# Kernel tuning notes

Measured on AMD Instinct MI355X. Metric: run time of the kernel, lower is better.

Reference implementation:

```python
import jax, jax.numpy as jnp
import numpy as np

B, S, IN, HID = 16, 4096, 512, 512
NH = 4
HD = HID // NH            # 128
NA = 4 * 2                # num_attractors*2 = 8 codes per head
EPS = 1e-5


def _ln(x, g, b):
    m = jnp.mean(x, axis=-1, keepdims=True)
    v = jnp.mean((x - m) ** 2, axis=-1, keepdims=True)
    return (x - m) * jax.lax.rsqrt(v + EPS) * g + b


def setup_inputs() -> dict:
    key = jax.random.key(0)
    ks = jax.random.split(key, 16)
    d = {
        "x": jax.random.normal(ks[0], (B, S, IN), jnp.float32),
        "norm_g": jnp.ones((IN,), jnp.float32),
        "norm_b": jnp.zeros((IN,), jnp.float32),
        # per-head MLP (stacked over head axis h)
        "hW1": jax.random.normal(ks[1], (NH, IN, 2 * HD), jnp.float32) / np.sqrt(IN).astype(np.float32),
        "hb1": jnp.zeros((NH, 2 * HD), jnp.float32),
        "hln_g": jnp.ones((NH, 2 * HD), jnp.float32),
        "hln_b": jnp.zeros((NH, 2 * HD), jnp.float32),
        "hW2": jax.random.normal(ks[2], (NH, 2 * HD, HD), jnp.float32) / np.sqrt(2 * HD).astype(np.float32),
        "hb2": jnp.zeros((NH, HD), jnp.float32),
        # attractor codebooks, dynamics, gates
        "attractors": jax.random.normal(ks[3], (NH, NA, HD), jnp.float32) / np.sqrt(HD).astype(np.float32),
        "dynamics": jnp.eye(HD, dtype=jnp.float32)[None] + 0.05 * jax.random.normal(ks[4], (NH, HD, HD), jnp.float32),
        "gW": jax.random.normal(ks[5], (NH, IN), jnp.float32) / np.sqrt(IN).astype(np.float32),
        "gb": jnp.zeros((NH,), jnp.float32),
        # output MLP
        "oW1": jax.random.normal(ks[6], (HID, HID), jnp.float32) / np.sqrt(HID).astype(np.float32),
        "ob1": jnp.zeros((HID,), jnp.float32),
        "oln_g": jnp.ones((HID,), jnp.float32),
        "oln_b": jnp.zeros((HID,), jnp.float32),
        "oW2": jax.random.normal(ks[7], (HID, IN), jnp.float32) / np.sqrt(HID).astype(np.float32),
        "ob2": jnp.zeros((IN,), jnp.float32),
    }
    return d


def reference(x, norm_g, norm_b, hW1, hb1, hln_g, hln_b, hW2, hb2,
              attractors, dynamics, gW, gb, oW1, ob1, oln_g, oln_b, oW2, ob2):
    xn = _ln(x, norm_g, norm_b)
    # per-head MLP (dropout is identity in eval): [B,S,NH,2HD] -> [B,S,NH,HD]
    h = jnp.einsum("bsi,hio->bsho", xn, hW1) + hb1
    h = jax.nn.gelu(_ln(h, hln_g, hln_b), approximate=False)
    state = jnp.einsum("bsho,hod->bshd", h, hW2) + hb2
    # cdist to tiny codebook via ||s||^2 + ||a||^2 - 2 s.a (matches torch.cdist matmul mode)
    s2 = jnp.sum(state * state, axis=-1, keepdims=True)          # [B,S,NH,1]
    a2 = jnp.sum(attractors * attractors, axis=-1)               # [NH,NA]
    sa = jnp.einsum("bshd,had->bsha", state, attractors)         # [B,S,NH,NA]
    dists = jnp.sqrt(jnp.maximum(s2 + a2 - 2.0 * sa, 0.0))
    attn = jax.nn.softmax(-dists / np.sqrt(HD).astype(np.float32), axis=-1)
    attr_infl = jnp.einsum("bsha,had->bshd", attn, attractors)
    dyn = jnp.einsum("bshd,hde->bshe", state, dynamics)
    gate = jax.nn.sigmoid(jnp.einsum("bsi,hi->bsh", xn, gW) + gb)[..., None]
    head_out = state + gate * 0.1 * (attr_infl - state + jnp.tanh(dyn))
    combined = head_out.reshape(*head_out.shape[:2], HID)        # concat heads
    o = combined @ oW1 + ob1
    o = jax.nn.gelu(_ln(o, oln_g, oln_b), approximate=False)
    o = o @ oW2 + ob2
    return xn + o
```

## Files before the change

### kernel.cpp

```cpp
#include <hip/hip_runtime.h>

typedef unsigned short u16;
typedef __bf16 bf16x8 __attribute__((ext_vector_type(8)));
typedef short  s16x8  __attribute__((ext_vector_type(8)));
typedef float  f32x4  __attribute__((ext_vector_type(4)));

template <bool B, class T, class F> struct cond_t { using type = T; };
template <class T, class F> struct cond_t<false, T, F> { using type = F; };
template <typename T>
__device__ auto probe_mfma(int)
    -> decltype(__builtin_amdgcn_mfma_f32_16x16x32_bf16(T{}, T{}, f32x4{}, 0, 0, 0), (char)0);
template <typename T> __device__ short probe_mfma(...);
using frag_t = typename cond_t<sizeof(probe_mfma<bf16x8>(0)) == 1, bf16x8, s16x8>::type;
#define MFMA(a, b, c) __builtin_amdgcn_mfma_f32_16x16x32_bf16((a), (b), (c), 0, 0, 0)

__device__ __forceinline__ float bf2f(u16 u) {
  unsigned int x = ((unsigned int)u) << 16; float f; __builtin_memcpy(&f, &x, 4); return f;
}
__device__ __forceinline__ u16 f2bf(float f) {
  unsigned int x; __builtin_memcpy(&x, &f, 4);
  x += 0x7fffu + ((x >> 16) & 1u);
  return (u16)(x >> 16);
}
__device__ __forceinline__ float fast_rcp(float x) { return __builtin_amdgcn_rcpf(x); }
__device__ __forceinline__ float tanh_fast(float x) {
  float t = __expf(2.0f * x);
  return 1.0f - 2.0f * fast_rcp(1.0f + t);
}
__device__ __forceinline__ float gelu_f(float x) {
  float x3 = x * x * x;
  return 0.5f * x * (1.0f + tanh_fast(0.7978845608028654f * x + 0.035677408136300125f * x3));
}
__device__ __forceinline__ float sigmoid_fast(float x) {
  return fast_rcp(1.0f + __expf(-x));
}

__global__ __launch_bounds__(256) void k_tr(const float* __restrict__ src, u16* __restrict__ dst,
                                            int batch, int K, int N) {
  long KN = (long)K * N;
  long total = (long)batch * KN;
  for (long i = (long)blockIdx.x * blockDim.x + threadIdx.x; i < total;
       i += (long)gridDim.x * blockDim.x) {
    long b = i / KN; long rem = i - b * KN;
    long n = rem / K; long k = rem - n * K;
    dst[i] = f2bf(src[b * KN + k * N + n]);
  }
}

__global__ __launch_bounds__(256) void k1_ln_gate(
    const float* __restrict__ x, const float* __restrict__ ng, const float* __restrict__ nb,
    const float* __restrict__ gW, const float* __restrict__ gb,
    u16* __restrict__ xn, float* __restrict__ gate) {
  const int lane = threadIdx.x & 63;
  const long t = (long)blockIdx.x * 4 + (threadIdx.x >> 6);
  float4 a0 = *(const float4*)(x + t * 512 + lane * 8);
  float4 a1 = *(const float4*)(x + t * 512 + lane * 8 + 4);
  float f[8] = {a0.x, a0.y, a0.z, a0.w, a1.x, a1.y, a1.z, a1.w};
  float s = 0.f, ss = 0.f;
#pragma unroll
  for (int j = 0; j < 8; j++) { s += f[j]; ss += f[j] * f[j]; }
#pragma unroll
  for (int m = 1; m < 64; m <<= 1) { s += __shfl_xor(s, m); ss += __shfl_xor(ss, m); }
  const float mean = s * (1.0f / 512.0f);
  const float rstd = rsqrtf(ss * (1.0f / 512.0f) - mean * mean + 1e-5f);
  float xf[8];
  union { uint4 q; u16 u[8]; } st;
#pragma unroll
  for (int j = 0; j < 8; j++) {
    xf[j] = (f[j] - mean) * rstd * ng[lane * 8 + j] + nb[lane * 8 + j];
    st.u[j] = f2bf(xf[j]);
  }
  *(uint4*)(xn + t * 512 + lane * 8) = st.q;
  for (int h = 0; h < 4; h++) {
    float p = 0.f;
#pragma unroll
    for (int j = 0; j < 8; j++) p += xf[j] * gW[h * 512 + lane * 8 + j];
#pragma unroll
    for (int m = 1; m < 64; m <<= 1) p += __shfl_xor(p, m);
    if (lane == 0) gate[t * 4 + h] = sigmoid_fast(p + gb[h]);
  }
}

__global__ __launch_bounds__(256, 1) void k2_head(
    const u16* __restrict__ xn, const u16* __restrict__ hW1t, const float* __restrict__ hb1,
    const float* __restrict__ hlng, const float* __restrict__ hlnb,
    const u16* __restrict__ hW2t, const float* __restrict__ hb2,
    const float* __restrict__ attr, const u16* __restrict__ dynT,
    const float* __restrict__ gate, u16* __restrict__ outC) {
  __shared__ __align__(16) char smem[44032];
  u16* sA  = (u16*)(smem);
  u16* sB  = (u16*)(smem + 5120);
  u16* sH  = (u16*)(smem);
  u16* sB2 = (u16*)(smem + 33792);
  u16* sSt = (u16*)(smem);
  float* sAttrF = (float*)(smem + 17408);
  float* sA2    = (float*)(smem + 21504);

  const int tid = threadIdx.x;
  const int lane = tid & 63, wv = tid >> 6, q = lane >> 4, l15 = lane & 15;
  const int h = blockIdx.y;
  const long t0 = (long)blockIdx.x * 64;
  const f32x4 vz = {0.f, 0.f, 0.f, 0.f};

  f32x4 acc[16];
#pragma unroll
  for (int i = 0; i < 16; i++) acc[i] = vz;
  const int arow = tid >> 2, ako = (tid & 3) * 8;

  for (int kb = 0; kb < 512; kb += 32) {
    *(uint4*)&sA[arow * 40 + ako] = *(const uint4*)&xn[(t0 + arow) * 512 + kb + ako];
#pragma unroll
    for (int i = 0; i < 4; i++) {
      int c = tid + 256 * i, r = c >> 2, ko = (c & 3) * 8;
      *(uint4*)&sB[r * 40 + ko] = *(const uint4*)&hW1t[((long)h * 256 + r) * 512 + kb + ko];
    }
    __syncthreads();
    frag_t af = *(const frag_t*)&sA[(wv * 16 + l15) * 40 + q * 8];
#pragma unroll
    for (int nt = 0; nt < 16; nt++) {
      frag_t bf = *(const frag_t*)&sB[(nt * 16 + l15) * 40 + q * 8];
      acc[nt] = MFMA(af, bf, acc[nt]);
    }
    __syncthreads();
  }

  {
    float bb[16], cg[16], cb[16];
#pragma unroll
    for (int nt = 0; nt < 16; nt++) {
      int col = nt * 16 + l15;
      bb[nt] = hb1[h * 256 + col];
      cg[nt] = hlng[h * 256 + col];
      cb[nt] = hlnb[h * 256 + col];
    }
#pragma unroll
    for (int r = 0; r < 4; r++) {
      float s = 0.f, ss = 0.f;
#pragma unroll
      for (int nt = 0; nt < 16; nt++) { float v = acc[nt][r] + bb[nt]; s += v; ss += v * v; }
#pragma unroll
      for (int m = 1; m < 16; m <<= 1) { s += __shfl_xor(s, m); ss += __shfl_xor(ss, m); }
      float mean = s * (1.f / 256.f);
      float rstd = rsqrtf(ss * (1.f / 256.f) - mean * mean + 1e-5f);
      int row = wv * 16 + q * 4 + r;
#pragma unroll
      for (int nt = 0; nt < 16; nt++) {
        float v = (acc[nt][r] + bb[nt] - mean) * rstd * cg[nt] + cb[nt];
        sH[row * 264 + nt * 16 + l15] = f2bf(gelu_f(v));
      }
    }
  }
  __syncthreads();

  f32x4 acc2[8];
#pragma unroll
  for (int i = 0; i < 8; i++) acc2[i] = vz;
  for (int kb = 0; kb < 256; kb += 32) {
#pragma unroll
    for (int i = 0; i < 2; i++) {
      int c = tid + 256 * i, r = c >> 2, ko = (c & 3) * 8;
      *(uint4*)&sB2[r * 40 + ko] = *(const uint4*)&hW2t[((long)h * 128 + r) * 256 + kb + ko];
    }
    __syncthreads();
    frag_t af = *(const frag_t*)&sH[(wv * 16 + l15) * 264 + kb + q * 8];
#pragma unroll
    for (int nt = 0; nt < 8; nt++) {
      frag_t bf = *(const frag_t*)&sB2[(nt * 16 + l15) * 40 + q * 8];
      acc2[nt] = MFMA(af, bf, acc2[nt]);
    }
    __syncthreads();
  }
#pragma unroll
  for (int nt = 0; nt < 8; nt++) {
    float b2 = hb2[h * 128 + nt * 16 + l15];
#pragma unroll
    for (int r = 0; r < 4; r++) acc2[nt][r] += b2;
  }

#pragma unroll
  for (int nt = 0; nt < 8; nt++)
#pragma unroll
    for (int r = 0; r < 4; r++)
      sSt[(wv * 16 + q * 4 + r) * 136 + nt * 16 + l15] = f2bf(acc2[nt][r]);
#pragma unroll
  for (int i = 0; i < 4; i++) { int c = tid + 256 * i; sAttrF[c] = attr[h * 1024 + c]; }
  __syncthreads();
  if (tid < 64) {
    int a = tid >> 3, j = tid & 7;
    float s = 0.f;
#pragma unroll
    for (int d2 = 0; d2 < 16; d2++) { float v = sAttrF[a * 128 + j * 16 + d2]; s += v * v; }
#pragma unroll
    for (int m = 1; m < 8; m <<= 1) s += __shfl_xor(s, m);
    if (j == 0) sA2[a] = s;
  }
  __syncthreads();

  f32x4 dacc[8];
#pragma unroll
  for (int i = 0; i < 8; i++) dacc[i] = vz;
  for (int kb = 0; kb < 128; kb += 32) {
#pragma unroll
    for (int i = 0; i < 2; i++) {
      int c = tid + 256 * i, r = c >> 2, ko = (c & 3) * 8;
      *(uint4*)&sB2[r * 40 + ko] = *(const uint4*)&dynT[((long)h * 128 + r) * 128 + kb + ko];
    }
    __syncthreads();
    frag_t af = *(const frag_t*)&sSt[(wv * 16 + l15) * 136 + kb + q * 8];
#pragma unroll
    for (int nt = 0; nt < 8; nt++) {
      frag_t bf = *(const frag_t*)&sB2[(nt * 16 + l15) * 40 + q * 8];
      dacc[nt] = MFMA(af, bf, dacc[nt]);
    }
    __syncthreads();
  }

  const float dscale = 0.088388347648318447f;
#pragma unroll
  for (int r = 0; r < 4; r++) {
    const long t = t0 + wv * 16 + q * 4 + r;
    float s2v = 0.f;
#pragma unroll
    for (int nt = 0; nt < 8; nt++) s2v += acc2[nt][r] * acc2[nt][r];
#pragma unroll
    for (int m = 1; m < 16; m <<= 1) s2v += __shfl_xor(s2v, m);
    float lg[8]; float mx = -3.0e38f;
#pragma unroll
    for (int a = 0; a < 8; a++) {
      float sa = 0.f;
#pragma unroll
      for (int nt = 0; nt < 8; nt++) sa += acc2[nt][r] * sAttrF[a * 128 + nt * 16 + l15];
#pragma unroll
      for (int m = 1; m < 16; m <<= 1) sa += __shfl_xor(sa, m);
      float dist = sqrtf(fmaxf(s2v + sA2[a] - 2.0f * sa, 0.0f));
      lg[a] = -dist * dscale;
      mx = fmaxf(mx, lg[a]);
    }
    float den = 0.f;
#pragma unroll
    for (int a = 0; a < 8; a++) { lg[a] = __expf(lg[a] - mx); den += lg[a]; }
    const float rden = fast_rcp(den);
    const float g01 = gate[t * 4 + h] * 0.1f;
#pragma unroll
    for (int nt = 0; nt < 8; nt++) {
      int col = nt * 16 + l15;
      float ai = 0.f;
#pragma unroll
      for (int a = 0; a < 8; a++) ai += lg[a] * sAttrF[a * 128 + col];
      ai *= rden;
      float stv = acc2[nt][r];
      float ho = stv + g01 * (ai - stv + tanh_fast(dacc[nt][r]));
      outC[t * 1024 + h * 128 + col] = f2bf(ho);
    }
  }
}

__global__ __launch_bounds__(256, 1) void k3_mlp1(
    const u16* __restrict__ inp, const u16* __restrict__ oW1t,
    const float* __restrict__ ob1, const float* __restrict__ olng, const float* __restrict__ olnb,
    u16* __restrict__ outp) {
  __shared__ __align__(16) char smem[46080];
  u16* sA = (u16*)smem;
  u16* sB = (u16*)(smem + 5120);
  const int tid = threadIdx.x, lane = tid & 63, wv = tid >> 6, q = lane >> 4, l15 = lane & 15;
  const long t0 = (long)blockIdx.x * 64;
  const f32x4 vz = {0.f, 0.f, 0.f, 0.f};
  f32x4 acc[32];
#pragma unroll
  for (int i = 0; i < 32; i++) acc[i] = vz;
  const int arow = tid >> 2, ako = (tid & 3) * 8;
  for (int kb = 0; kb < 512; kb += 32) {
    *(uint4*)&sA[arow * 40 + ako] = *(const uint4*)&inp[(t0 + arow) * 1024 + kb + ako];
#pragma unroll
    for (int i = 0; i < 8; i++) {
      int c = tid + 256 * i, r = c >> 2, ko = (c & 3) * 8;
      *(uint4*)&sB[r * 40 + ko] = *(const uint4*)&oW1t[(long)r * 512 + kb + ko];
    }
    __syncthreads();
    frag_t af = *(const frag_t*)&sA[(wv * 16 + l15) * 40 + q * 8];
#pragma unroll
    for (int nt = 0; nt < 32; nt++) {
      frag_t bf = *(const frag_t*)&sB[(nt * 16 + l15) * 40 + q * 8];
      acc[nt] = MFMA(af, bf, acc[nt]);
    }
    __syncthreads();
  }
  float bb[32];
#pragma unroll
  for (int nt = 0; nt < 32; nt++) bb[nt] = ob1[nt * 16 + l15];
#pragma unroll
  for (int r = 0; r < 4; r++) {
    float s = 0.f, ss = 0.f;
#pragma unroll
    for (int nt = 0; nt < 32; nt++) { float v = acc[nt][r] + bb[nt]; s += v; ss += v * v; }
#pragma unroll
    for (int m = 1; m < 16; m <<= 1) { s += __shfl_xor(s, m); ss += __shfl_xor(ss, m); }
    float mean = s * (1.f / 512.f);
    float rstd = rsqrtf(ss * (1.f / 512.f) - mean * mean + 1e-5f);
    const long t = t0 + wv * 16 + q * 4 + r;
#pragma unroll
    for (int nt = 0; nt < 32; nt++) {
      int col = nt * 16 + l15;
      float v = (acc[nt][r] + bb[nt] - mean) * rstd * olng[col] + olnb[col];
      outp[t * 1024 + col] = f2bf(gelu_f(v));
    }
  }
}

__global__ __launch_bounds__(256, 1) void k4_mlp2(
    const u16* __restrict__ inp, const u16* __restrict__ oW2t,
    const float* __restrict__ ob2, const u16* __restrict__ xn,
    float* __restrict__ outp) {
  __shared__ __align__(16) char smem[46080];
  u16* sA = (u16*)smem;
  u16* sB = (u16*)(smem + 5120);
  const int tid = threadIdx.x, lane = tid & 63, wv = tid >> 6, q = lane >> 4, l15 = lane & 15;
  const long t0 = (long)blockIdx.x * 64;
  const f32x4 vz = {0.f, 0.f, 0.f, 0.f};
  f32x4 acc[32];
#pragma unroll
  for (int i = 0; i < 32; i++) acc[i] = vz;
  const int arow = tid >> 2, ako = (tid & 3) * 8;
  for (int kb = 0; kb < 512; kb += 32) {
    *(uint4*)&sA[arow * 40 + ako] = *(const uint4*)&inp[(t0 + arow) * 1024 + kb + ako];
#pragma unroll
    for (int i = 0; i < 8; i++) {
      int c = tid + 256 * i, r = c >> 2, ko = (c & 3) * 8;
      *(uint4*)&sB[r * 40 + ko] = *(const uint4*)&oW2t[(long)r * 512 + kb + ko];
    }
    __syncthreads();
    frag_t af = *(const frag_t*)&sA[(wv * 16 + l15) * 40 + q * 8];
#pragma unroll
    for (int nt = 0; nt < 32; nt++) {
      frag_t bf = *(const frag_t*)&sB[(nt * 16 + l15) * 40 + q * 8];
      acc[nt] = MFMA(af, bf, acc[nt]);
    }
    __syncthreads();
  }
#pragma unroll
  for (int r = 0; r < 4; r++) {
    const long t = t0 + wv * 16 + q * 4 + r;
#pragma unroll
    for (int nt = 0; nt < 32; nt++) {
      int col = nt * 16 + l15;
      float v = acc[nt][r] + ob2[col] + bf2f(xn[t * 512 + col]);
      outp[t * 512 + col] = v;
    }
  }
}

extern "C" void kernel_launch(void* const* d_in, const int* in_sizes, int n_in,
                              void* d_out, int out_size, void* d_ws, size_t ws_size,
                              hipStream_t stream) {
  const float* x    = (const float*)d_in[0];
  const float* ng   = (const float*)d_in[1];
  const float* nbp  = (const float*)d_in[2];
  const float* hW1  = (const float*)d_in[3];
  const float* hb1  = (const float*)d_in[4];
  const float* hlng = (const float*)d_in[5];
  const float* hlnb = (const float*)d_in[6];
  const float* hW2  = (const float*)d_in[7];
  const float* hb2  = (const float*)d_in[8];
  const float* attr = (const float*)d_in[9];
  const float* dyn  = (const float*)d_in[10];
  const float* gW   = (const float*)d_in[11];
  const float* gb   = (const float*)d_in[12];
  const float* oW1  = (const float*)d_in[13];
  const float* ob1  = (const float*)d_in[14];
  const float* olng = (const float*)d_in[15];
  const float* olnb = (const float*)d_in[16];
  const float* oW2  = (const float*)d_in[17];
  const float* ob2  = (const float*)d_in[18];

  char* ws = (char*)d_ws;
  u16*   xn   = (u16*)ws;
  float* gate = (float*)(ws + 67108864);
  u16*   wT   = (u16*)(ws + 68157440);
  u16* hW1t = wT;
  u16* hW2t = wT + 524288;
  u16* dynT = wT + 655360;
  u16* oW1t = wT + 720896;
  u16* oW2t = wT + 983040;

  k_tr<<<512, 256, 0, stream>>>(hW1, hW1t, 4, 512, 256);
  k_tr<<<128, 256, 0, stream>>>(hW2, hW2t, 4, 256, 128);
  k_tr<<<64, 256, 0, stream>>>(dyn, dynT, 4, 128, 128);
  k_tr<<<256, 256, 0, stream>>>(oW1, oW1t, 1, 512, 512);
  k_tr<<<256, 256, 0, stream>>>(oW2, oW2t, 1, 512, 512);

  k1_ln_gate<<<16384, 256, 0, stream>>>(x, ng, nbp, gW, gb, xn, gate);

  u16* cb = (u16*)d_out;
  k2_head<<<dim3(1024, 4), 256, 0, stream>>>(xn, hW1t, hb1, hlng, hlnb, hW2t, hb2,
                                             attr, dynT, gate, cb);
  k3_mlp1<<<1024, 256, 0, stream>>>(cb, oW1t, ob1, olng, olnb, cb + 512);
  k4_mlp2<<<1024, 256, 0, stream>>>(cb + 512, oW2t, ob2, xn, (float*)d_out);
}
```

Measured before the change: 848.8 us.

## Restructure head kernel with async LDS double-buffering, swizzled layouts and MFMA attractor math

Rewrites the per-head kernel. The first GEMM now uses global_load_lds double buffering with XOR-swizzled shared memory and a 2x2 wave tiling, and LayerNorm statistics are combined across waves through shared memory. The second and dynamics GEMMs read B fragments straight from global memory, dropping shared staging and barriers. The attractor dot products and the softmax-weighted sum move onto MFMA using padded bf16 codebooks. Shared memory drops and launch bounds allow 4 blocks per CU for occupancy, at the cost of bf16 rounding in the attractor path and uncached global B-fragment loads.

```diff
diff --git a/kernel.cpp b/kernel.cpp
--- a/kernel.cpp
+++ b/kernel.cpp
@@ -33,6 +33,12 @@
 }
 __device__ __forceinline__ float sigmoid_fast(float x) {
   return fast_rcp(1.0f + __expf(-x));
+}
+
+typedef const __attribute__((address_space(1))) void gvoid_t;
+typedef __attribute__((address_space(3))) void lvoid_t;
+__device__ __forceinline__ void gl16(const u16* g, char* l) {
+  __builtin_amdgcn_global_load_lds((gvoid_t*)g, (lvoid_t*)l, 16, 0, 0);
 }
 
 __global__ __launch_bounds__(256) void k_tr(const float* __restrict__ src, u16* __restrict__ dst,
@@ -81,94 +87,151 @@
   }
 }
 
-__global__ __launch_bounds__(256, 1) void k2_head(
+__global__ __launch_bounds__(256, 4) void k2_head(
     const u16* __restrict__ xn, const u16* __restrict__ hW1t, const float* __restrict__ hb1,
     const float* __restrict__ hlng, const float* __restrict__ hlnb,
     const u16* __restrict__ hW2t, const float* __restrict__ hb2,
     const float* __restrict__ attr, const u16* __restrict__ dynT,
     const float* __restrict__ gate, u16* __restrict__ outC) {
-  __shared__ __align__(16) char smem[44032];
-  u16* sA  = (u16*)(smem);
-  u16* sB  = (u16*)(smem + 5120);
-  u16* sH  = (u16*)(smem);
-  u16* sB2 = (u16*)(smem + 33792);
-  u16* sSt = (u16*)(smem);
-  float* sAttrF = (float*)(smem + 17408);
-  float* sA2    = (float*)(smem + 21504);
-
+  __shared__ __align__(16) char smem[40960];
   const int tid = threadIdx.x;
   const int lane = tid & 63, wv = tid >> 6, q = lane >> 4, l15 = lane & 15;
+  const int wr = wv >> 1, wc = wv & 1;
   const int h = blockIdx.y;
   const long t0 = (long)blockIdx.x * 64;
   const f32x4 vz = {0.f, 0.f, 0.f, 0.f};
 
-  f32x4 acc[16];
-#pragma unroll
-  for (int i = 0; i < 16; i++) acc[i] = vz;
-  const int arow = tid >> 2, ako = (tid & 3) * 8;
-
-  for (int kb = 0; kb < 512; kb += 32) {
-    *(uint4*)&sA[arow * 40 + ako] = *(const uint4*)&xn[(t0 + arow) * 512 + kb + ako];
-#pragma unroll
-    for (int i = 0; i < 4; i++) {
-      int c = tid + 256 * i, r = c >> 2, ko = (c & 3) * 8;
-      *(uint4*)&sB[r * 40 + ko] = *(const uint4*)&hW1t[((long)h * 256 + r) * 512 + kb + ko];
+  const int pr = lane >> 3, posp = lane & 7;
+  const int pos = posp ^ pr;
+  const int rl = pr * 2 + (pos >> 2), ck = pos & 3;
+  const u16* gA = xn + ((size_t)(t0 + wv * 16 + rl) << 9) + ck * 8;
+  const u16* gB = hW1t + ((((size_t)h * 256) + wv * 64 + rl) << 9) + ck * 8;
+  char* const lA = smem + wv * 1024;
+  char* const lB = smem + 8192 + wv * 4096;
+
+  int afo[2], bfo[8];
+#pragma unroll
+  for (int i = 0; i < 2; i++) {
+    int row = wr * 32 + i * 16 + l15;
+    afo[i] = (row >> 1) * 128 + (((((row & 1) << 2) | q) ^ ((row >> 1) & 7)) << 4);
+  }
+#pragma unroll
+  for (int nt = 0; nt < 8; nt++) {
+    int row = wc * 128 + nt * 16 + l15;
+    bfo[nt] = (row >> 1) * 128 + (((((row & 1) << 2) | q) ^ ((row >> 1) & 7)) << 4);
+  }
+
+  f32x4 acc[2][8];
+#pragma unroll
+  for (int i = 0; i < 2; i++)
+#pragma unroll
+    for (int nt = 0; nt < 8; nt++) acc[i][nt] = vz;
+
+#define STAGE1(buf)                                     \
+  {                                                     \
+    gl16(gA, lA + (buf) * 4096);                        \
+    gl16(gB, lB + (buf) * 16384);                       \
+    gl16(gB + 8192, lB + (buf) * 16384 + 1024);         \
+    gl16(gB + 16384, lB + (buf) * 16384 + 2048);        \
+    gl16(gB + 24576, lB + (buf) * 16384 + 3072);        \
+    gA += 32; gB += 32;                                 \
+  }
+
+  STAGE1(0);
+  __syncthreads();
+#pragma unroll 2
+  for (int k = 0; k < 16; ++k) {
+    const int cur = k & 1;
+    if (k < 15) STAGE1(cur ^ 1);
+    const char* Ab = smem + cur * 4096;
+    const char* Bb = smem + 8192 + cur * 16384;
+    frag_t a0 = *(const frag_t*)(Ab + afo[0]);
+    frag_t a1 = *(const frag_t*)(Ab + afo[1]);
+#pragma unroll
+    for (int nt = 0; nt < 8; nt++) {
+      frag_t bf = *(const frag_t*)(Bb + bfo[nt]);
+      acc[0][nt] = MFMA(a0, bf, acc[0][nt]);
+      acc[1][nt] = MFMA(a1, bf, acc[1][nt]);
     }
     __syncthreads();
-    frag_t af = *(const frag_t*)&sA[(wv * 16 + l15) * 40 + q * 8];
-#pragma unroll
-    for (int nt = 0; nt < 16; nt++) {
-      frag_t bf = *(const frag_t*)&sB[(nt * 16 + l15) * 40 + q * 8];
-      acc[nt] = MFMA(af, bf, acc[nt]);
-    }
-    __syncthreads();
-  }
-
-  {
-    float bb[16], cg[16], cb[16];
-#pragma unroll
-    for (int nt = 0; nt < 16; nt++) {
-      int col = nt * 16 + l15;
-      bb[nt] = hb1[h * 256 + col];
-      cg[nt] = hlng[h * 256 + col];
-      cb[nt] = hlnb[h * 256 + col];
-    }
+  }
+#undef STAGE1
+
+  float bb[8], cg[8], cbv[8];
+#pragma unroll
+  for (int nt = 0; nt < 8; nt++) {
+    int c = h * 256 + wc * 128 + nt * 16 + l15;
+    bb[nt] = hb1[c]; cg[nt] = hlng[c]; cbv[nt] = hlnb[c];
+  }
+  float* sLN = (float*)(smem + 32768);
+#pragma unroll
+  for (int i = 0; i < 2; i++)
 #pragma unroll
     for (int r = 0; r < 4; r++) {
       float s = 0.f, ss = 0.f;
 #pragma unroll
-      for (int nt = 0; nt < 16; nt++) { float v = acc[nt][r] + bb[nt]; s += v; ss += v * v; }
+      for (int nt = 0; nt < 8; nt++) { float v = acc[i][nt][r] + bb[nt]; s += v; ss = fmaf(v, v, ss); }
 #pragma unroll
       for (int m = 1; m < 16; m <<= 1) { s += __shfl_xor(s, m); ss += __shfl_xor(ss, m); }
+      if (l15 == 0) {
+        int row = wr * 32 + i * 16 + q * 4 + r;
+        sLN[row * 4 + wc * 2] = s; sLN[row * 4 + wc * 2 + 1] = ss;
+      }
+    }
+  float* sA2 = (float*)(smem + 37888);
+  if (wv == 0) {
+    int a = lane >> 3, jj = lane & 7;
+    float s = 0.f;
+#pragma unroll
+    for (int d2 = 0; d2 < 16; d2++) { float v = attr[h * 1024 + a * 128 + jj * 16 + d2]; s = fmaf(v, v, s); }
+#pragma unroll
+    for (int m = 1; m < 8; m <<= 1) s += __shfl_xor(s, m);
+    if (jj == 0) sA2[a] = s;
+  }
+#pragma unroll
+  for (int j = 0; j < 8; j++) {
+    int idx = tid * 8 + j, ar = idx >> 7, d = idx & 127;
+    u16 v = (ar < 8) ? f2bf(attr[h * 1024 + ar * 128 + d]) : (u16)0;
+    *(u16*)(smem + 33792 + ar * 256 + ((2 * d) ^ ((ar & 7) << 4))) = v;
+  }
+  __syncthreads();
+#pragma unroll
+  for (int i = 0; i < 2; i++)
+#pragma unroll
+    for (int r = 0; r < 4; r++) {
+      int row = wr * 32 + i * 16 + q * 4 + r;
+      float s = sLN[row * 4] + sLN[row * 4 + 2], ss = sLN[row * 4 + 1] + sLN[row * 4 + 3];
       float mean = s * (1.f / 256.f);
       float rstd = rsqrtf(ss * (1.f / 256.f) - mean * mean + 1e-5f);
-      int row = wv * 16 + q * 4 + r;
-#pragma unroll
-      for (int nt = 0; nt < 16; nt++) {
-        float v = (acc[nt][r] + bb[nt] - mean) * rstd * cg[nt] + cb[nt];
-        sH[row * 264 + nt * 16 + l15] = f2bf(gelu_f(v));
+      float mr = -mean * rstd;
+#pragma unroll
+      for (int nt = 0; nt < 8; nt++) {
+        float v = fmaf(acc[i][nt][r] + bb[nt], rstd, mr);
+        v = fmaf(v, cg[nt], cbv[nt]);
+        int col = wc * 128 + nt * 16 + l15;
+        *(u16*)(smem + row * 512 + ((2 * col) ^ ((row & 7) << 4))) = f2bf(gelu_f(v));
       }
     }
-  }
   __syncthreads();
 
   f32x4 acc2[8];
 #pragma unroll
-  for (int i = 0; i < 8; i++) acc2[i] = vz;
-  for (int kb = 0; kb < 256; kb += 32) {
-#pragma unroll
-    for (int i = 0; i < 2; i++) {
-      int c = tid + 256 * i, r = c >> 2, ko = (c & 3) * 8;
-      *(uint4*)&sB2[r * 40 + ko] = *(const uint4*)&hW2t[((long)h * 128 + r) * 256 + kb + ko];
-    }
-    __syncthreads();
-    frag_t af = *(const frag_t*)&sH[(wv * 16 + l15) * 264 + kb + q * 8];
-#pragma unroll
-    for (int nt = 0; nt < 8; nt++) {
-      frag_t bf = *(const frag_t*)&sB2[(nt * 16 + l15) * 40 + q * 8];
-      acc2[nt] = MFMA(af, bf, acc2[nt]);
-    }
-    __syncthreads();
+  for (int nt = 0; nt < 8; nt++) acc2[nt] = vz;
+  {
+    const int rb2 = (wv * 16 + l15) * 512, sw2 = (l15 & 7) << 4;
+    const u16* pB2[8];
+#pragma unroll
+    for (int nt = 0; nt < 8; nt++)
+      pB2[nt] = hW2t + ((((size_t)h * 128) + nt * 16 + l15) << 8) + q * 8;
+#pragma unroll
+    for (int kb = 0; kb < 256; kb += 32) {
+      frag_t af = *(const frag_t*)(smem + rb2 + ((kb * 2 + q * 16) ^ sw2));
+#pragma unroll
+      for (int nt = 0; nt < 8; nt++) {
+        frag_t bf = *(const frag_t*)(pB2[nt] + kb);
+        acc2[nt] = MFMA(af, bf, acc2[nt]);
+      }
+    }
   }
 #pragma unroll
   for (int nt = 0; nt < 8; nt++) {
@@ -176,81 +239,107 @@
 #pragma unroll
     for (int r = 0; r < 4; r++) acc2[nt][r] += b2;
   }
+  float s2v[4];
+#pragma unroll
+  for (int r = 0; r < 4; r++) {
+    float s = 0.f;
+#pragma unroll
+    for (int nt = 0; nt < 8; nt++) s = fmaf(acc2[nt][r], acc2[nt][r], s);
+#pragma unroll
+    for (int m = 1; m < 16; m <<= 1) s += __shfl_xor(s, m);
+    s2v[r] = s;
+  }
+  __syncthreads();
 
 #pragma unroll
   for (int nt = 0; nt < 8; nt++)
 #pragma unroll
+    for (int r = 0; r < 4; r++) {
+      int row = wv * 16 + q * 4 + r, col = nt * 16 + l15;
+      *(u16*)(smem + row * 256 + ((2 * col) ^ ((row & 7) << 4))) = f2bf(acc2[nt][r]);
+    }
+#pragma unroll
+  for (int j = 0; j < 16; j++) {
+    int idx = tid * 16 + j, row = idx >> 5, kk = idx & 31;
+    u16 v = (kk < 8) ? f2bf(attr[h * 1024 + kk * 128 + row]) : (u16)0;
+    *(u16*)(smem + 20480 + row * 64 + ((2 * kk) ^ ((row & 3) << 4))) = v;
+  }
+  __syncthreads();
+
+  f32x4 dacc[8], sacc = vz;
+#pragma unroll
+  for (int nt = 0; nt < 8; nt++) dacc[nt] = vz;
+  {
+    const int rb3 = (wv * 16 + l15) * 256, sw3 = (l15 & 7) << 4;
+    const u16* pD[8];
+#pragma unroll
+    for (int nt = 0; nt < 8; nt++)
+      pD[nt] = dynT + ((((size_t)h * 128) + nt * 16 + l15) << 7) + q * 8;
+#pragma unroll
+    for (int kb = 0; kb < 128; kb += 32) {
+      const int ko = (kb * 2 + q * 16) ^ sw3;
+      frag_t af = *(const frag_t*)(smem + rb3 + ko);
+      frag_t ab = *(const frag_t*)(smem + 33792 + l15 * 256 + ko);
+      sacc = MFMA(af, ab, sacc);
+#pragma unroll
+      for (int nt = 0; nt < 8; nt++) {
+        frag_t bf = *(const frag_t*)(pD[nt] + kb);
+        dacc[nt] = MFMA(af, bf, dacc[nt]);
+      }
+    }
+  }
+
+  const float dscale = 0.088388347648318447f;
+  float g01[4];
+#pragma unroll
+  for (int r = 0; r < 4; r++)
+    g01[r] = gate[(t0 + wv * 16 + q * 4 + r) * 4 + h] * 0.1f;
+  const float a2l = (l15 < 8) ? ((const float*)(smem + 37888))[l15] : 0.f;
+#pragma unroll
+  for (int r = 0; r < 4; r++) {
+    float lg = -3.0e38f;
+    if (l15 < 8) {
+      float d2 = fmaxf(fmaf(-2.f, sacc[r], s2v[r] + a2l), 0.f);
+      lg = -sqrtf(d2) * dscale;
+    }
+    float mx = lg;
+#pragma unroll
+    for (int m = 1; m < 16; m <<= 1) mx = fmaxf(mx, __shfl_xor(mx, m));
+    float p = __expf(lg - mx), den = p;
+#pragma unroll
+    for (int m = 1; m < 16; m <<= 1) den += __shfl_xor(den, m);
+    p *= fast_rcp(den);
+    int row = wv * 16 + q * 4 + r;
+    *(u16*)(smem + 16384 + row * 64 + ((2 * l15) ^ ((row & 3) << 4))) = f2bf(p);
+  }
+
+#pragma unroll
+  for (int nt = 0; nt < 8; nt++)
+#pragma unroll
     for (int r = 0; r < 4; r++)
-      sSt[(wv * 16 + q * 4 + r) * 136 + nt * 16 + l15] = f2bf(acc2[nt][r]);
-#pragma unroll
-  for (int i = 0; i < 4; i++) { int c = tid + 256 * i; sAttrF[c] = attr[h * 1024 + c]; }
-  __syncthreads();
-  if (tid < 64) {
-    int a = tid >> 3, j = tid & 7;
-    float s = 0.f;
-#pragma unroll
-    for (int d2 = 0; d2 < 16; d2++) { float v = sAttrF[a * 128 + j * 16 + d2]; s += v * v; }
-#pragma unroll
-    for (int m = 1; m < 8; m <<= 1) s += __shfl_xor(s, m);
-    if (j == 0) sA2[a] = s;
-  }
-  __syncthreads();
-
-  f32x4 dacc[8];
-#pragma unroll
-  for (int i = 0; i < 8; i++) dacc[i] = vz;
-  for (int kb = 0; kb < 128; kb += 32) {
-#pragma unroll
-    for (int i = 0; i < 2; i++) {
-      int c = tid + 256 * i, r = c >> 2, ko = (c & 3) * 8;
-      *(uint4*)&sB2[r * 40 + ko] = *(const uint4*)&dynT[((long)h * 128 + r) * 128 + kb + ko];
-    }
-    __syncthreads();
-    frag_t af = *(const frag_t*)&sSt[(wv * 16 + l15) * 136 + kb + q * 8];
+      dacc[nt][r] = acc2[nt][r] + g01[r] * (tanh_fast(dacc[nt][r]) - acc2[nt][r]);
+
+  f32x4 aacc[8];
+#pragma unroll
+  for (int nt = 0; nt < 8; nt++) aacc[nt] = vz;
+  {
+    const int rowa = wv * 16 + l15;
+    frag_t ap = *(const frag_t*)(smem + 16384 + rowa * 64 + ((q * 16) ^ ((l15 & 3) << 4)));
 #pragma unroll
     for (int nt = 0; nt < 8; nt++) {
-      frag_t bf = *(const frag_t*)&sB2[(nt * 16 + l15) * 40 + q * 8];
-      dacc[nt] = MFMA(af, bf, dacc[nt]);
-    }
-    __syncthreads();
-  }
-
-  const float dscale = 0.088388347648318447f;
+      int rowb = nt * 16 + l15;
+      frag_t bf = *(const frag_t*)(smem + 20480 + rowb * 64 + ((q * 16) ^ ((l15 & 3) << 4)));
+      aacc[nt] = MFMA(ap, bf, aacc[nt]);
+    }
+  }
+
 #pragma unroll
   for (int r = 0; r < 4; r++) {
     const long t = t0 + wv * 16 + q * 4 + r;
-    float s2v = 0.f;
-#pragma unroll
-    for (int nt = 0; nt < 8; nt++) s2v += acc2[nt][r] * acc2[nt][r];
-#pragma unroll
-    for (int m = 1; m < 16; m <<= 1) s2v += __shfl_xor(s2v, m);
-    float lg[8]; float mx = -3.0e38f;
-#pragma unroll
-    for (int a = 0; a < 8; a++) {
-      float sa = 0.f;
-#pragma unroll
-      for (int nt = 0; nt < 8; nt++) sa += acc2[nt][r] * sAttrF[a * 128 + nt * 16 + l15];
-#pragma unroll
-      for (int m = 1; m < 16; m <<= 1) sa += __shfl_xor(sa, m);
-      float dist = sqrtf(fmaxf(s2v + sA2[a] - 2.0f * sa, 0.0f));
-      lg[a] = -dist * dscale;
-      mx = fmaxf(mx, lg[a]);
-    }
-    float den = 0.f;
-#pragma unroll
-    for (int a = 0; a < 8; a++) { lg[a] = __expf(lg[a] - mx); den += lg[a]; }
-    const float rden = fast_rcp(den);
-    const float g01 = gate[t * 4 + h] * 0.1f;
 #pragma unroll
     for (int nt = 0; nt < 8; nt++) {
       int col = nt * 16 + l15;
-      float ai = 0.f;
-#pragma unroll
-      for (int a = 0; a < 8; a++) ai += lg[a] * sAttrF[a * 128 + col];
-      ai *= rden;
-      float stv = acc2[nt][r];
-      float ho = stv + g01 * (ai - stv + tanh_fast(dacc[nt][r]));
-      outC[t * 1024 + h * 128 + col] = f2bf(ho);
+      outC[t * 1024 + h * 128 + col] = f2bf(dacc[nt][r] + g01[r] * aacc[nt][r]);
     }
   }
 }
```

New measurement: 838.2 us. No clear change (-1.3%).
